# Optimization experiments

Measured on AMD Instinct MI355X. Metric: run time of the kernel, lower is better.

Reference implementation:

```python
import jax, jax.numpy as jnp
import numpy as np

L, B, D_MODEL, N_STATE = 512, 32, 256, 16
DT_RANK = 16          # ceil(d_model / 16)
D_INNER = D_MODEL     # EXPAND = 1 (required for code self-consistency)


def setup_inputs() -> dict:
    key = jax.random.key(0)
    ks = jax.random.split(key, 6)
    return {
        "position_features": jax.random.normal(ks[0], (L, B, D_MODEL), jnp.float32),
        "flow_features": jax.random.normal(ks[1], (L, B, D_MODEL), jnp.float32),
        "h_state": jnp.zeros((B, D_INNER, N_STATE), jnp.float32),
        "x_proj_w": jax.random.normal(ks[2], (DT_RANK + 2 * N_STATE, D_INNER), jnp.float32) / np.sqrt(D_INNER).astype(np.float32),
        "dt_proj_w": jax.random.normal(ks[3], (D_INNER, DT_RANK), jnp.float32) / np.sqrt(DT_RANK).astype(np.float32),
        "dt_proj_b": jax.random.normal(ks[4], (D_INNER,), jnp.float32) * 0.01,
        "A_log": jnp.log(jnp.broadcast_to(jnp.arange(1, N_STATE + 1, dtype=jnp.float32), (D_INNER, N_STATE))),
        "D_param": jnp.ones((D_INNER,), jnp.float32),
        "out_proj_w": jax.random.normal(ks[5], (D_MODEL, D_INNER), jnp.float32) / np.sqrt(D_INNER).astype(np.float32),
    }


def _forward(position_features, flow_features, h_state,
             x_proj_w, dt_proj_w, dt_proj_b, A_log, D_param, out_proj_w):
    # permute (L, B, d) -> (B, L, d), matching forward()'s permute(1,0,2)
    u = jnp.transpose(position_features, (1, 0, 2))      # (b, l, d_in)
    flow = jnp.transpose(flow_features, (1, 0, 2))       # (b, l, d_in)

    # input-dependent delta, B, C from flow features
    x_dbl = flow @ x_proj_w.T                            # (b, l, dt_rank + 2n)
    delta, Bm, Cm = jnp.split(x_dbl, [DT_RANK, DT_RANK + N_STATE], axis=-1)
    delta = jax.nn.softplus(delta @ dt_proj_w.T + dt_proj_b)   # (b, l, d_in)

    A = -jnp.exp(A_log)                                  # (d_in, n)
    deltaA = jnp.exp(jnp.einsum('bld,dn->bldn', delta, A))         # (b,l,d,n)
    deltaB_u = jnp.einsum('bld,bln,bld->bldn', delta, Bm, u)       # (b,l,d,n)

    # sequential selective scan over l via lax.scan
    dA_t = jnp.swapaxes(deltaA, 0, 1)                    # (l, b, d, n)
    dBu_t = jnp.swapaxes(deltaB_u, 0, 1)                 # (l, b, d, n)
    C_t = jnp.swapaxes(Cm, 0, 1)                         # (l, b, n)

    def step(h, xs):
        dA, dBu, c = xs
        h = dA * h + dBu                                 # (b, d, n)
        y = jnp.einsum('bdn,bn->bd', h, c)               # (b, d)
        return h, y

    h_final, ys = jax.lax.scan(step, h_state, (dA_t, dBu_t, C_t))
    y = jnp.swapaxes(ys, 0, 1)                           # (b, l, d_in)
    y = y + u * D_param                                  # skip connection

    out = y @ out_proj_w.T                               # (b, l, d_model)
    return out.reshape(out.shape[0], -1), h_final        # flatten(1)


def reference(position_features, flow_features, h_state,
              x_proj_w, dt_proj_w, dt_proj_b, A_log, D_param, out_proj_w):
    return _forward(position_features, flow_features, h_state,
                    x_proj_w, dt_proj_w, dt_proj_b, A_log, D_param, out_proj_w)
```

## Files before the change

kernel.cpp:

```cpp
#include <hip/hip_runtime.h>
#include <hip/hip_bf16.h>

#define LL 512
#define BB 32
#define DD 256
#define NS 16
#define RK 16
#define CH4 32
#define LC4 16
#define DT4 16

typedef __attribute__((ext_vector_type(8))) short bf16x8;
typedef __attribute__((ext_vector_type(8))) _Float16 f16x8;
typedef __attribute__((ext_vector_type(4))) float f32x4;

#define LD16(dst, src, off) { \
  float4 _v0 = *reinterpret_cast<const float4*>(&(src)[(off)]); \
  float4 _v1 = *reinterpret_cast<const float4*>(&(src)[(off)+4]); \
  float4 _v2 = *reinterpret_cast<const float4*>(&(src)[(off)+8]); \
  float4 _v3 = *reinterpret_cast<const float4*>(&(src)[(off)+12]); \
  dst[0]=_v0.x; dst[1]=_v0.y; dst[2]=_v0.z; dst[3]=_v0.w; \
  dst[4]=_v1.x; dst[5]=_v1.y; dst[6]=_v1.z; dst[7]=_v1.w; \
  dst[8]=_v2.x; dst[9]=_v2.y; dst[10]=_v2.z; dst[11]=_v2.w; \
  dst[12]=_v3.x; dst[13]=_v3.y; dst[14]=_v3.z; dst[15]=_v3.w; }

static __device__ __forceinline__ unsigned short f2bf(float x) {
    __hip_bfloat16 h = __float2bfloat16(x);
    return *reinterpret_cast<unsigned short*>(&h);
}

static __device__ __forceinline__ f16x8 ld_cvt_f16(const float* p) {
    float4 lo = *reinterpret_cast<const float4*>(p);
    float4 hi = *reinterpret_cast<const float4*>(p + 4);
    f16x8 r;
    r[0] = (_Float16)lo.x; r[1] = (_Float16)lo.y; r[2] = (_Float16)lo.z; r[3] = (_Float16)lo.w;
    r[4] = (_Float16)hi.x; r[5] = (_Float16)hi.y; r[6] = (_Float16)hi.z; r[7] = (_Float16)hi.w;
    return r;
}

__global__ __launch_bounds__(256) void k0_wbf(
    const float* __restrict__ W, unsigned short* __restrict__ Wbf)
{
    int i = (blockIdx.x * 256 + threadIdx.x) * 4;
    float4 v = *reinterpret_cast<const float4*>(&W[i]);
    ushort4 o;
    o.x = f2bf(v.x); o.y = f2bf(v.y); o.z = f2bf(v.z); o.w = f2bf(v.w);
    *reinterpret_cast<ushort4*>(&Wbf[i]) = o;
}

__global__ __launch_bounds__(256) void k1a_xdbl(
    const float* __restrict__ flow,
    const float* __restrict__ x_proj_w,
    float* __restrict__ xdbl)
{
    int wave = threadIdx.x >> 6;
    int lane = threadIdx.x & 63;
    int rl = lane & 15, kb = lane >> 4;
    int arow = blockIdx.x * 64 + wave * 16 + rl;
    int b = arow >> 9, l = arow & 511;
    const float* abase = &flow[(l * BB + b) * DD];

    f32x4 acc[3] = {};
    #pragma unroll
    for (int ks = 0; ks < 8; ++ks) {
        int k0 = ks * 32 + kb * 8;
        f16x8 af = ld_cvt_f16(abase + k0);
        #pragma unroll
        for (int j = 0; j < 3; ++j) {
            f16x8 bf = ld_cvt_f16(&x_proj_w[(j * 16 + rl) * DD + k0]);
            acc[j] = __builtin_amdgcn_mfma_f32_16x16x32_f16(af, bf, acc[j], 0, 0, 0);
        }
    }
    int row_out = blockIdx.x * 64 + wave * 16 + kb * 4;
    #pragma unroll
    for (int j = 0; j < 3; ++j)
        #pragma unroll
        for (int reg = 0; reg < 4; ++reg)
            xdbl[(size_t)(row_out + reg) * 48 + j * 16 + rl] = acc[j][reg];
}

__global__ __launch_bounds__(256) void k1b_proj(
    const float* __restrict__ xdbl,
    const float* __restrict__ dt_w,
    const float* __restrict__ dt_b,
    float* __restrict__ delta,
    float* __restrict__ Bm,
    float* __restrict__ Cm)
{
    __shared__ float sx[32 * 48];
    int tid = threadIdx.x;
    int row0 = blockIdx.x * 32;

    {
        int i4 = tid;
        *reinterpret_cast<float4*>(&sx[i4 * 4]) =
            *reinterpret_cast<const float4*>(&xdbl[(size_t)row0 * 48 + i4 * 4]);
        i4 = tid + 256;
        if (i4 < 384)
            *reinterpret_cast<float4*>(&sx[i4 * 4]) =
                *reinterpret_cast<const float4*>(&xdbl[(size_t)row0 * 48 + i4 * 4]);
    }
    __syncthreads();

    #pragma unroll
    for (int jj = 0; jj < 2; ++jj) {
        int idx = tid + jj * 256;
        int r = idx >> 4, c = idx & 15;
        Bm[(size_t)(row0 + r) * NS + c] = sx[r * 48 + RK + c];
        Cm[(size_t)(row0 + r) * NS + c] = sx[r * 48 + RK + NS + c];
    }

    float wreg[RK];
    #pragma unroll
    for (int k = 0; k < RK; k += 4) {
        float4 v = *reinterpret_cast<const float4*>(&dt_w[tid * RK + k]);
        wreg[k] = v.x; wreg[k + 1] = v.y; wreg[k + 2] = v.z; wreg[k + 3] = v.w;
    }
    float bias = dt_b[tid];
    for (int r = 0; r < 32; ++r) {
        const float* srow = &sx[r * 48];
        float s = bias;
        #pragma unroll
        for (int k = 0; k < RK; ++k) s = fmaf(srow[k], wreg[k], s);
        float sp = fmaxf(s, 0.f) + log1pf(__expf(-fabsf(s)));
        delta[(size_t)(row0 + r) * DD + tid] = sp;
    }
}

__global__ __launch_bounds__(512) void k2_fused(
    const float* __restrict__ u_pos,
    const float* __restrict__ h0,
    const float* __restrict__ A_log,
    const float* __restrict__ Dp,
    const float* __restrict__ delta,
    const float* __restrict__ Bm,
    const float* __restrict__ Cm,
    unsigned short* __restrict__ ybf,
    float* __restrict__ h_out)
{
    extern __shared__ float smem[];
    float* lap = smem;
    float* lhp = smem + NS * CH4 * DT4;

    int tid = threadIdx.x;
    int b  = blockIdx.x >> 4;
    int dt = blockIdx.x & 15;
    int dl = tid & 15, c = tid >> 4;
    int d  = dt * DT4 + dl;
    int l0 = c * LC4;

    float a[NS];
    #pragma unroll
    for (int n = 0; n < NS; n += 4) {
        float4 v = *reinterpret_cast<const float4*>(&A_log[d * NS + n]);
        a[n]     = -__expf(v.x) * 1.44269504f;
        a[n + 1] = -__expf(v.y) * 1.44269504f;
        a[n + 2] = -__expf(v.z) * 1.44269504f;
        a[n + 3] = -__expf(v.w) * 1.44269504f;
    }

    const float* dp = delta + ((size_t)b * LL + l0) * DD + d;
    const float* up = u_pos + ((size_t)l0 * BB + b) * DD + d;
    const float* Bp = Bm + ((size_t)b * LL + l0) * NS;
    const float* Cp = Cm + ((size_t)b * LL + l0) * NS;

    float h[NS], ap[NS];
    #pragma unroll
    for (int n = 0; n < NS; ++n) { h[n] = 0.f; ap[n] = 1.f; }

    for (int l = 0; l < LC4; l += 2) {
        float d0 = dp[l * DD],        d1 = dp[(l + 1) * DD];
        float u0 = up[l * BB * DD],   u1 = up[(l + 1) * BB * DD];
        float B0[NS], B1[NS];
        LD16(B0, Bp, l * NS);
        LD16(B1, Bp, (l + 1) * NS);
        float du0 = d0 * u0, du1 = d1 * u1;
        #pragma unroll
        for (int n = 0; n < NS; ++n) {
            float dA = exp2f(d0 * a[n]);
            ap[n] *= dA;
            h[n] = fmaf(dA, h[n], du0 * B0[n]);
        }
        #pragma unroll
        for (int n = 0; n < NS; ++n) {
            float dA = exp2f(d1 * a[n]);
            ap[n] *= dA;
            h[n] = fmaf(dA, h[n], du1 * B1[n]);
        }
    }
    #pragma unroll
    for (int n = 0; n < NS; ++n) {
        lap[n * (CH4 * DT4) + c * DT4 + dl] = ap[n];
        lhp[n * (CH4 * DT4) + c * DT4 + dl] = h[n];
    }
    __syncthreads();

    if (tid < DT4 * NS) {
        int dl2 = tid & 15, n2 = tid >> 4;
        float s = h0[((size_t)b * DD + dt * DT4 + dl2) * NS + n2];
        #pragma unroll 4
        for (int c2 = 0; c2 < CH4; ++c2) {
            int idx = n2 * (CH4 * DT4) + c2 * DT4 + dl2;
            float apv = lap[idx];
            float hpv = lhp[idx];
            lap[idx] = s;
            s = fmaf(apv, s, hpv);
        }
        h_out[((size_t)b * DD + dt * DT4 + dl2) * NS + n2] = s;
    }
    __syncthreads();

    #pragma unroll
    for (int n = 0; n < NS; ++n)
        h[n] = lap[n * (CH4 * DT4) + c * DT4 + dl];
    float Dd = Dp[d];
    unsigned short* yp = ybf + ((size_t)b * LL + l0) * DD + d;

    for (int l = 0; l < LC4; l += 2) {
        float d0 = dp[l * DD],        d1 = dp[(l + 1) * DD];
        float u0 = up[l * BB * DD],   u1 = up[(l + 1) * BB * DD];
        float B0[NS], B1[NS], C0[NS], C1[NS];
        LD16(B0, Bp, l * NS);
        LD16(B1, Bp, (l + 1) * NS);
        LD16(C0, Cp, l * NS);
        LD16(C1, Cp, (l + 1) * NS);

        float du0 = d0 * u0, du1 = d1 * u1;
        float acc0 = 0.f, acc1 = 0.f;
        #pragma unroll
        for (int n = 0; n < NS; ++n) {
            float dA = exp2f(d0 * a[n]);
            h[n] = fmaf(dA, h[n], du0 * B0[n]);
            acc0 = fmaf(h[n], C0[n], acc0);
        }
        #pragma unroll
        for (int n = 0; n < NS; ++n) {
            float dA = exp2f(d1 * a[n]);
            h[n] = fmaf(dA, h[n], du1 * B1[n]);
            acc1 = fmaf(h[n], C1[n], acc1);
        }
        yp[l * DD]       = f2bf(fmaf(u0, Dd, acc0));
        yp[(l + 1) * DD] = f2bf(fmaf(u1, Dd, acc1));
    }
}

__global__ __launch_bounds__(256) void k3_mfma(
    const unsigned short* __restrict__ Ybf,
    const unsigned short* __restrict__ Wbf,
    float* __restrict__ Out)
{
    int wave = threadIdx.x >> 6;
    int lane = threadIdx.x & 63;
    int row0 = (blockIdx.x >> 1) * 64 + (wave >> 1) * 32;
    int col0 = (blockIdx.x & 1) * 128 + (wave & 1) * 64;
    int rl = lane & 15, kb = lane >> 4;

    f32x4 acc[2][4] = {};
    bf16x8 af[2], bf[4], afn[2], bfn[4];

    #pragma unroll
    for (int i = 0; i < 2; ++i)
        af[i] = *reinterpret_cast<const bf16x8*>(&Ybf[(size_t)(row0 + i * 16 + rl) * DD + kb * 8]);
    #pragma unroll
    for (int j = 0; j < 4; ++j)
        bf[j] = *reinterpret_cast<const bf16x8*>(&Wbf[(size_t)(col0 + j * 16 + rl) * DD + kb * 8]);

    #pragma unroll
    for (int ks = 0; ks < 8; ++ks) {
        int kn = (ks + 1) * 32 + kb * 8;
        if (ks < 7) {
            #pragma unroll
            for (int i = 0; i < 2; ++i)
                afn[i] = *reinterpret_cast<const bf16x8*>(&Ybf[(size_t)(row0 + i * 16 + rl) * DD + kn]);
            #pragma unroll
            for (int j = 0; j < 4; ++j)
                bfn[j] = *reinterpret_cast<const bf16x8*>(&Wbf[(size_t)(col0 + j * 16 + rl) * DD + kn]);
        }
        #pragma unroll
        for (int i = 0; i < 2; ++i)
            #pragma unroll
            for (int j = 0; j < 4; ++j)
                acc[i][j] = __builtin_amdgcn_mfma_f32_16x16x32_bf16(af[i], bf[j], acc[i][j], 0, 0, 0);
        #pragma unroll
        for (int i = 0; i < 2; ++i) af[i] = afn[i];
        #pragma unroll
        for (int j = 0; j < 4; ++j) bf[j] = bfn[j];
    }

    #pragma unroll
    for (int i = 0; i < 2; ++i)
        #pragma unroll
        for (int j = 0; j < 4; ++j)
            #pragma unroll
            for (int reg = 0; reg < 4; ++reg)
                Out[(size_t)(row0 + i * 16 + kb * 4 + reg) * DD + col0 + j * 16 + rl] = acc[i][j][reg];
}

extern "C" void kernel_launch(void* const* d_in, const int* in_sizes, int n_in,
                              void* d_out, int out_size, void* d_ws, size_t ws_size,
                              hipStream_t stream) {
    const float* pos  = (const float*)d_in[0];
    const float* flow = (const float*)d_in[1];
    const float* h0   = (const float*)d_in[2];
    const float* xw   = (const float*)d_in[3];
    const float* dtw  = (const float*)d_in[4];
    const float* dtb  = (const float*)d_in[5];
    const float* alog = (const float*)d_in[6];
    const float* dpar = (const float*)d_in[7];
    const float* ow   = (const float*)d_in[8];

    float* out = (float*)d_out;

    float* ws    = (float*)d_ws;
    float* delta = ws;
    float* Bmw   = ws + 4194304;
    float* Cmw   = ws + 4456448;
    unsigned short* ybf = (unsigned short*)(ws + 4718592);
    unsigned short* wbf = (unsigned short*)(ws + 6815744);
    float* xdbl  = ws + 6848512;

    float* h_out = out + 32 * 512 * 256;

    k0_wbf  <<<64,  256, 0, stream>>>(ow, wbf);
    k1a_xdbl<<<256, 256, 0, stream>>>(flow, xw, xdbl);
    k1b_proj<<<512, 256, 0, stream>>>(xdbl, dtw, dtb, delta, Bmw, Cmw);
    k2_fused<<<512, 512, 65536, stream>>>(pos, h0, alog, dpar, delta, Bmw, Cmw, ybf, h_out);
    k3_mfma <<<512, 256, 0, stream>>>(ybf, wbf, out);
}
```

Before: 184.7 us.

## Split chunked scan into local pass, carry pass, and correction pass; fuse x/dt projections

The fused two-pass chunked scan is replaced by three kernels. The first scans each chunk once with zero initial state, emitting partial outputs, cumulative delta sums and final chunk states. The second propagates carries across chunks using exp2 of the summed delta. The third adds the carry contribution to each output in a fully parallel pass, where exp(a*S)*C*h_in is summed over n. This removes the second sequential recurrence pass, but adds full-size fp32 intermediate buffers (ypart, cumulative delta, per-chunk states) that increase memory traffic. The x_proj and dt_proj steps are merged into one kernel that uses MFMA for the rank-16 projection. The A table is precomputed once, and the output GEMM tile is halved to launch more blocks.

```diff
diff --git a/kernel.cpp b/kernel.cpp
--- a/kernel.cpp
+++ b/kernel.cpp
@@ -6,9 +6,8 @@
 #define DD 256
 #define NS 16
 #define RK 16
-#define CH4 32
-#define LC4 16
-#define DT4 16
+#define CH 32
+#define LC 16
 
 typedef __attribute__((ext_vector_type(8))) short bf16x8;
 typedef __attribute__((ext_vector_type(8))) _Float16 f16x8;
@@ -48,15 +47,28 @@
     *reinterpret_cast<ushort4*>(&Wbf[i]) = o;
 }
 
-__global__ __launch_bounds__(256) void k1a_xdbl(
+__global__ __launch_bounds__(256) void k0_atab(
+    const float* __restrict__ A_log, float* __restrict__ atab)
+{
+    int i = blockIdx.x * 256 + threadIdx.x;
+    atab[i] = -__expf(A_log[i]) * 1.44269504f;
+}
+
+__global__ __launch_bounds__(256) void k1_fused(
     const float* __restrict__ flow,
-    const float* __restrict__ x_proj_w,
-    float* __restrict__ xdbl)
-{
+    const float* __restrict__ xw,
+    const float* __restrict__ dtw,
+    const float* __restrict__ dtb,
+    float* __restrict__ delta,
+    float* __restrict__ Bm,
+    float* __restrict__ Cm)
+{
+    __shared__ float sx16[4][16][17];
     int wave = threadIdx.x >> 6;
     int lane = threadIdx.x & 63;
     int rl = lane & 15, kb = lane >> 4;
-    int arow = blockIdx.x * 64 + wave * 16 + rl;
+    int rowbase = blockIdx.x * 64 + wave * 16;
+    int arow = rowbase + rl;
     int b = arow >> 9, l = arow & 511;
     const float* abase = &flow[(l * BB + b) * DD];
 
@@ -67,181 +79,161 @@
         f16x8 af = ld_cvt_f16(abase + k0);
         #pragma unroll
         for (int j = 0; j < 3; ++j) {
-            f16x8 bf = ld_cvt_f16(&x_proj_w[(j * 16 + rl) * DD + k0]);
-            acc[j] = __builtin_amdgcn_mfma_f32_16x16x32_f16(af, bf, acc[j], 0, 0, 0);
-        }
-    }
-    int row_out = blockIdx.x * 64 + wave * 16 + kb * 4;
-    #pragma unroll
-    for (int j = 0; j < 3; ++j)
-        #pragma unroll
-        for (int reg = 0; reg < 4; ++reg)
-            xdbl[(size_t)(row_out + reg) * 48 + j * 16 + rl] = acc[j][reg];
-}
-
-__global__ __launch_bounds__(256) void k1b_proj(
-    const float* __restrict__ xdbl,
-    const float* __restrict__ dt_w,
-    const float* __restrict__ dt_b,
+            f16x8 bfr = ld_cvt_f16(&xw[(j * 16 + rl) * DD + k0]);
+            acc[j] = __builtin_amdgcn_mfma_f32_16x16x32_f16(af, bfr, acc[j], 0, 0, 0);
+        }
+    }
+    #pragma unroll
+    for (int reg = 0; reg < 4; ++reg) {
+        int row = rowbase + kb * 4 + reg;
+        Bm[(size_t)row * NS + rl] = acc[1][reg];
+        Cm[(size_t)row * NS + rl] = acc[2][reg];
+        sx16[wave][kb * 4 + reg][rl] = acc[0][reg];
+    }
+    __syncthreads();
+
+    f16x8 a2;
+    if (kb < 2) {
+        #pragma unroll
+        for (int j = 0; j < 8; ++j)
+            a2[j] = (_Float16)sx16[wave][rl][kb * 8 + j];
+    } else {
+        #pragma unroll
+        for (int j = 0; j < 8; ++j) a2[j] = (_Float16)0.f;
+    }
+
+    #pragma unroll 4
+    for (int m = 0; m < 16; ++m) {
+        f16x8 b2;
+        if (kb < 2) {
+            float4 lo = *reinterpret_cast<const float4*>(&dtw[(m * 16 + rl) * RK + kb * 8]);
+            float4 hi = *reinterpret_cast<const float4*>(&dtw[(m * 16 + rl) * RK + kb * 8 + 4]);
+            b2[0] = (_Float16)lo.x; b2[1] = (_Float16)lo.y; b2[2] = (_Float16)lo.z; b2[3] = (_Float16)lo.w;
+            b2[4] = (_Float16)hi.x; b2[5] = (_Float16)hi.y; b2[6] = (_Float16)hi.z; b2[7] = (_Float16)hi.w;
+        } else {
+            #pragma unroll
+            for (int j = 0; j < 8; ++j) b2[j] = (_Float16)0.f;
+        }
+        f32x4 acc2 = {};
+        acc2 = __builtin_amdgcn_mfma_f32_16x16x32_f16(a2, b2, acc2, 0, 0, 0);
+        int d = m * 16 + rl;
+        float bias = dtb[d];
+        #pragma unroll
+        for (int reg = 0; reg < 4; ++reg) {
+            float s = acc2[reg] + bias;
+            float sp = fmaxf(s, 0.f) + log1pf(__expf(-fabsf(s)));
+            delta[(size_t)(rowbase + kb * 4 + reg) * DD + d] = sp;
+        }
+    }
+}
+
+__global__ __launch_bounds__(512) void k2A(
+    const float* __restrict__ u_pos,
+    const float* __restrict__ atab,
+    const float* __restrict__ Dp,
     float* __restrict__ delta,
-    float* __restrict__ Bm,
-    float* __restrict__ Cm)
-{
-    __shared__ float sx[32 * 48];
-    int tid = threadIdx.x;
-    int row0 = blockIdx.x * 32;
-
-    {
-        int i4 = tid;
-        *reinterpret_cast<float4*>(&sx[i4 * 4]) =
-            *reinterpret_cast<const float4*>(&xdbl[(size_t)row0 * 48 + i4 * 4]);
-        i4 = tid + 256;
-        if (i4 < 384)
-            *reinterpret_cast<float4*>(&sx[i4 * 4]) =
-                *reinterpret_cast<const float4*>(&xdbl[(size_t)row0 * 48 + i4 * 4]);
-    }
-    __syncthreads();
-
-    #pragma unroll
-    for (int jj = 0; jj < 2; ++jj) {
-        int idx = tid + jj * 256;
-        int r = idx >> 4, c = idx & 15;
-        Bm[(size_t)(row0 + r) * NS + c] = sx[r * 48 + RK + c];
-        Cm[(size_t)(row0 + r) * NS + c] = sx[r * 48 + RK + NS + c];
-    }
-
-    float wreg[RK];
-    #pragma unroll
-    for (int k = 0; k < RK; k += 4) {
-        float4 v = *reinterpret_cast<const float4*>(&dt_w[tid * RK + k]);
-        wreg[k] = v.x; wreg[k + 1] = v.y; wreg[k + 2] = v.z; wreg[k + 3] = v.w;
-    }
-    float bias = dt_b[tid];
-    for (int r = 0; r < 32; ++r) {
-        const float* srow = &sx[r * 48];
-        float s = bias;
-        #pragma unroll
-        for (int k = 0; k < RK; ++k) s = fmaf(srow[k], wreg[k], s);
-        float sp = fmaxf(s, 0.f) + log1pf(__expf(-fabsf(s)));
-        delta[(size_t)(row0 + r) * DD + tid] = sp;
-    }
-}
-
-__global__ __launch_bounds__(512) void k2_fused(
-    const float* __restrict__ u_pos,
-    const float* __restrict__ h0,
-    const float* __restrict__ A_log,
-    const float* __restrict__ Dp,
-    const float* __restrict__ delta,
     const float* __restrict__ Bm,
     const float* __restrict__ Cm,
-    unsigned short* __restrict__ ybf,
-    float* __restrict__ h_out)
-{
-    extern __shared__ float smem[];
-    float* lap = smem;
-    float* lhp = smem + NS * CH4 * DT4;
-
+    float* __restrict__ ypart,
+    float* __restrict__ hfin,
+    float* __restrict__ sfin)
+{
     int tid = threadIdx.x;
     int b  = blockIdx.x >> 4;
     int dt = blockIdx.x & 15;
     int dl = tid & 15, c = tid >> 4;
-    int d  = dt * DT4 + dl;
-    int l0 = c * LC4;
+    int d  = dt * 16 + dl;
+    int l0 = c * LC;
 
     float a[NS];
-    #pragma unroll
-    for (int n = 0; n < NS; n += 4) {
-        float4 v = *reinterpret_cast<const float4*>(&A_log[d * NS + n]);
-        a[n]     = -__expf(v.x) * 1.44269504f;
-        a[n + 1] = -__expf(v.y) * 1.44269504f;
-        a[n + 2] = -__expf(v.z) * 1.44269504f;
-        a[n + 3] = -__expf(v.w) * 1.44269504f;
-    }
-
-    const float* dp = delta + ((size_t)b * LL + l0) * DD + d;
+    LD16(a, atab, d * NS);
+    float Dd = Dp[d];
+
+    float* dp = delta + ((size_t)b * LL + l0) * DD + d;
     const float* up = u_pos + ((size_t)l0 * BB + b) * DD + d;
     const float* Bp = Bm + ((size_t)b * LL + l0) * NS;
     const float* Cp = Cm + ((size_t)b * LL + l0) * NS;
-
-    float h[NS], ap[NS];
-    #pragma unroll
-    for (int n = 0; n < NS; ++n) { h[n] = 0.f; ap[n] = 1.f; }
-
-    for (int l = 0; l < LC4; l += 2) {
-        float d0 = dp[l * DD],        d1 = dp[(l + 1) * DD];
-        float u0 = up[l * BB * DD],   u1 = up[(l + 1) * BB * DD];
-        float B0[NS], B1[NS];
-        LD16(B0, Bp, l * NS);
-        LD16(B1, Bp, (l + 1) * NS);
-        float du0 = d0 * u0, du1 = d1 * u1;
+    float* yp = ypart + ((size_t)b * LL + l0) * DD + d;
+
+    float h[NS];
+    #pragma unroll
+    for (int n = 0; n < NS; ++n) h[n] = 0.f;
+    float s = 0.f;
+
+    for (int l = 0; l < LC; ++l) {
+        float dlt = dp[l * DD];
+        float uv  = up[l * BB * DD];
+        float Bv[NS], Cv[NS];
+        LD16(Bv, Bp, l * NS);
+        LD16(Cv, Cp, l * NS);
+        s += dlt;
+        float du = dlt * uv;
+        float acc = uv * Dd;
         #pragma unroll
         for (int n = 0; n < NS; ++n) {
-            float dA = exp2f(d0 * a[n]);
-            ap[n] *= dA;
-            h[n] = fmaf(dA, h[n], du0 * B0[n]);
-        }
-        #pragma unroll
-        for (int n = 0; n < NS; ++n) {
-            float dA = exp2f(d1 * a[n]);
-            ap[n] *= dA;
-            h[n] = fmaf(dA, h[n], du1 * B1[n]);
-        }
-    }
-    #pragma unroll
-    for (int n = 0; n < NS; ++n) {
-        lap[n * (CH4 * DT4) + c * DT4 + dl] = ap[n];
-        lhp[n * (CH4 * DT4) + c * DT4 + dl] = h[n];
-    }
-    __syncthreads();
-
-    if (tid < DT4 * NS) {
-        int dl2 = tid & 15, n2 = tid >> 4;
-        float s = h0[((size_t)b * DD + dt * DT4 + dl2) * NS + n2];
-        #pragma unroll 4
-        for (int c2 = 0; c2 < CH4; ++c2) {
-            int idx = n2 * (CH4 * DT4) + c2 * DT4 + dl2;
-            float apv = lap[idx];
-            float hpv = lhp[idx];
-            lap[idx] = s;
-            s = fmaf(apv, s, hpv);
-        }
-        h_out[((size_t)b * DD + dt * DT4 + dl2) * NS + n2] = s;
-    }
-    __syncthreads();
-
+            float dA = exp2f(dlt * a[n]);
+            h[n] = fmaf(dA, h[n], du * Bv[n]);
+            acc = fmaf(h[n], Cv[n], acc);
+        }
+        yp[l * DD] = acc;
+        dp[l * DD] = s;
+    }
+
+    size_t o = (((size_t)b * CH + c) * DD + d);
+    sfin[o] = s;
+    #pragma unroll
+    for (int n = 0; n < NS; n += 4)
+        *reinterpret_cast<float4*>(&hfin[o * NS + n]) =
+            make_float4(h[n], h[n+1], h[n+2], h[n+3]);
+}
+
+__global__ __launch_bounds__(256) void k2B(
+    const float* __restrict__ h0,
+    const float* __restrict__ atab,
+    const float* __restrict__ sfin,
+    float* __restrict__ hfin,
+    float* __restrict__ h_out)
+{
+    int t = blockIdx.x * 256 + threadIdx.x;
+    int n = t & 15, d = (t >> 4) & 255, b = t >> 12;
+    float an = atab[d * NS + n];
+    float s = h0[t];
+    for (int c = 0; c < CH; ++c) {
+        size_t o = ((size_t)b * CH + c) * DD + d;
+        float sf = sfin[o];
+        size_t oh = o * NS + n;
+        float hp = hfin[oh];
+        hfin[oh] = s;
+        s = fmaf(exp2f(an * sf), s, hp);
+    }
+    h_out[t] = s;
+}
+
+__global__ __launch_bounds__(256) void k2C(
+    const float* __restrict__ atab,
+    const float* __restrict__ Slocal,
+    const float* __restrict__ Cm,
+    const float* __restrict__ hfin,
+    const float* __restrict__ ypart,
+    unsigned short* __restrict__ ybf)
+{
+    int d = threadIdx.x;
+    int b = blockIdx.x >> 9;
+    int l = blockIdx.x & 511;
+    int c = l >> 4;
+
+    float a[NS], hin[NS], Cv[NS];
+    LD16(a, atab, d * NS);
+    LD16(hin, hfin, (((size_t)b * CH + c) * DD + d) * NS);
+    LD16(Cv, Cm, ((size_t)b * LL + l) * NS);
+
+    size_t idx = ((size_t)b * LL + l) * DD + d;
+    float sS = Slocal[idx];
+    float acc = ypart[idx];
     #pragma unroll
     for (int n = 0; n < NS; ++n)
-        h[n] = lap[n * (CH4 * DT4) + c * DT4 + dl];
-    float Dd = Dp[d];
-    unsigned short* yp = ybf + ((size_t)b * LL + l0) * DD + d;
-
-    for (int l = 0; l < LC4; l += 2) {
-        float d0 = dp[l * DD],        d1 = dp[(l + 1) * DD];
-        float u0 = up[l * BB * DD],   u1 = up[(l + 1) * BB * DD];
-        float B0[NS], B1[NS], C0[NS], C1[NS];
-        LD16(B0, Bp, l * NS);
-        LD16(B1, Bp, (l + 1) * NS);
-        LD16(C0, Cp, l * NS);
-        LD16(C1, Cp, (l + 1) * NS);
-
-        float du0 = d0 * u0, du1 = d1 * u1;
-        float acc0 = 0.f, acc1 = 0.f;
-        #pragma unroll
-        for (int n = 0; n < NS; ++n) {
-            float dA = exp2f(d0 * a[n]);
-            h[n] = fmaf(dA, h[n], du0 * B0[n]);
-            acc0 = fmaf(h[n], C0[n], acc0);
-        }
-        #pragma unroll
-        for (int n = 0; n < NS; ++n) {
-            float dA = exp2f(d1 * a[n]);
-            h[n] = fmaf(dA, h[n], du1 * B1[n]);
-            acc1 = fmaf(h[n], C1[n], acc1);
-        }
-        yp[l * DD]       = f2bf(fmaf(u0, Dd, acc0));
-        yp[(l + 1) * DD] = f2bf(fmaf(u1, Dd, acc1));
-    }
+        acc = fmaf(exp2f(a[n] * sS), Cv[n] * hin[n], acc);
+    ybf[idx] = f2bf(acc);
 }
 
 __global__ __launch_bounds__(256) void k3_mfma(
@@ -251,16 +243,14 @@
 {
     int wave = threadIdx.x >> 6;
     int lane = threadIdx.x & 63;
-    int row0 = (blockIdx.x >> 1) * 64 + (wave >> 1) * 32;
+    int row0 = (blockIdx.x >> 1) * 32 + (wave >> 1) * 16;
     int col0 = (blockIdx.x & 1) * 128 + (wave & 1) * 64;
     int rl = lane & 15, kb = lane >> 4;
 
-    f32x4 acc[2][4] = {};
-    bf16x8 af[2], bf[4], afn[2], bfn[4];
-
-    #pragma unroll
-    for (int i = 0; i < 2; ++i)
-        af[i] = *reinterpret_cast<const bf16x8*>(&Ybf[(size_t)(row0 + i * 16 + rl) * DD + kb * 8]);
+    f32x4 acc[4] = {};
+    bf16x8 af, bf[4], afn, bfn[4];
+
+    af = *reinterpret_cast<const bf16x8*>(&Ybf[(size_t)(row0 + rl) * DD + kb * 8]);
     #pragma unroll
     for (int j = 0; j < 4; ++j)
         bf[j] = *reinterpret_cast<const bf16x8*>(&Wbf[(size_t)(col0 + j * 16 + rl) * DD + kb * 8]);
@@ -269,31 +259,24 @@
     for (int ks = 0; ks < 8; ++ks) {
         int kn = (ks + 1) * 32 + kb * 8;
         if (ks < 7) {
-            #pragma unroll
-            for (int i = 0; i < 2; ++i)
-                afn[i] = *reinterpret_cast<const bf16x8*>(&Ybf[(size_t)(row0 + i * 16 + rl) * DD + kn]);
+            afn = *reinterpret_cast<const bf16x8*>(&Ybf[(size_t)(row0 + rl) * DD + kn]);
             #pragma unroll
             for (int j = 0; j < 4; ++j)
                 bfn[j] = *reinterpret_cast<const bf16x8*>(&Wbf[(size_t)(col0 + j * 16 + rl) * DD + kn]);
         }
         #pragma unroll
-        for (int i = 0; i < 2; ++i)
-            #pragma unroll
-            for (int j = 0; j < 4; ++j)
-                acc[i][j] = __builtin_amdgcn_mfma_f32_16x16x32_bf16(af[i], bf[j], acc[i][j], 0, 0, 0);
-        #pragma unroll
-        for (int i = 0; i < 2; ++i) af[i] = afn[i];
+        for (int j = 0; j < 4; ++j)
+            acc[j] = __builtin_amdgcn_mfma_f32_16x16x32_bf16(af, bf[j], acc[j], 0, 0, 0);
+        af = afn;
         #pragma unroll
         for (int j = 0; j < 4; ++j) bf[j] = bfn[j];
     }
 
     #pragma unroll
-    for (int i = 0; i < 2; ++i)
-        #pragma unroll
-        for (int j = 0; j < 4; ++j)
-            #pragma unroll
-            for (int reg = 0; reg < 4; ++reg)
-                Out[(size_t)(row0 + i * 16 + kb * 4 + reg) * DD + col0 + j * 16 + rl] = acc[i][j][reg];
+    for (int j = 0; j < 4; ++j)
+        #pragma unroll
+        for (int reg = 0; reg < 4; ++reg)
+            Out[(size_t)(row0 + kb * 4 + reg) * DD + col0 + j * 16 + rl] = acc[j][reg];
 }
 
 extern "C" void kernel_launch(void* const* d_in, const int* in_sizes, int n_in,
@@ -315,15 +298,20 @@
     float* delta = ws;
     float* Bmw   = ws + 4194304;
     float* Cmw   = ws + 4456448;
-    unsigned short* ybf = (unsigned short*)(ws + 4718592);
-    unsigned short* wbf = (unsigned short*)(ws + 6815744);
-    float* xdbl  = ws + 6848512;
+    float* ypart = ws + 4718592;
+    float* hfin  = ws + 8912896;
+    float* sfin  = ws + 13107200;
+    float* atab  = ws + 13369344;
+    unsigned short* ybf = (unsigned short*)(ws + 13373440);
+    unsigned short* wbf = (unsigned short*)(ws + 15470592);
 
     float* h_out = out + 32 * 512 * 256;
 
-    k0_wbf  <<<64,  256, 0, stream>>>(ow, wbf);
-    k1a_xdbl<<<256, 256, 0, stream>>>(flow, xw, xdbl);
-    k1b_proj<<<512, 256, 0, stream>>>(xdbl, dtw, dtb, delta, Bmw, Cmw);
-    k2_fused<<<512, 512, 65536, stream>>>(pos, h0, alog, dpar, delta, Bmw, Cmw, ybf, h_out);
-    k3_mfma <<<512, 256, 0, stream>>>(ybf, wbf, out);
-}
+    k0_wbf  <<<64,    256, 0, stream>>>(ow, wbf);
+    k0_atab <<<16,    256, 0, stream>>>(alog, atab);
+    k1_fused<<<256,   256, 0, stream>>>(flow, xw, dtw, dtb, delta, Bmw, Cmw);
+    k2A     <<<512,   512, 0, stream>>>(pos, atab, dpar, delta, Bmw, Cmw, ypart, hfin, sfin);
+    k2B     <<<512,   256, 0, stream>>>(h0, atab, sfin, hfin, h_out);
+    k2C     <<<16384, 256, 0, stream>>>(atab, delta, Cmw, hfin, ypart, ybf);
+    k3_mfma <<<1024,  256, 0, stream>>>(ybf, wbf, out);
+}
```

Result: slower. 226.5 us (+22.6%).
